# Kernel tuning notes

Measured on AMD Instinct MI355X. Metric: run time of the kernel, lower is better.

The kernel has to match this reference:

```python
import jax, jax.numpy as jnp
import numpy as np

N_NODES = 200000
N_EVENTS = 150000
MEM_DIM = 128
RAW_DIM = 128
TIME_DIM = 128
MSG_DIM = 2 * MEM_DIM + RAW_DIM + TIME_DIM  # 512, IdentityMessage out_channels


def setup_inputs() -> dict:
    key = jax.random.key(0)
    ks = jax.random.split(key, 10)
    memory = jax.random.normal(ks[0], (N_NODES, MEM_DIM), jnp.float32)
    last_update = jax.random.randint(ks[1], (N_NODES,), 0, 1000, jnp.int32)
    src = jax.random.randint(ks[2], (N_EVENTS,), 0, N_NODES, jnp.int32)
    dst = jax.random.randint(ks[3], (N_EVENTS,), 0, N_NODES, jnp.int32)
    t = jax.random.randint(ks[4], (N_EVENTS,), 0, 100000, jnp.int32)
    raw_msg = jax.random.normal(ks[5], (N_EVENTS, RAW_DIM), jnp.float32)
    time_w = jax.random.normal(ks[6], (TIME_DIM,), jnp.float32) * 0.05
    time_b = jax.random.normal(ks[7], (TIME_DIM,), jnp.float32) * 0.05
    W_ih = jax.random.normal(ks[8], (3 * MEM_DIM, MSG_DIM), jnp.float32) * (1.0 / np.sqrt(MSG_DIM))
    W_hh = jax.random.normal(ks[9], (3 * MEM_DIM, MEM_DIM), jnp.float32) * (1.0 / np.sqrt(MEM_DIM))
    b_ih = jnp.zeros((3 * MEM_DIM,), jnp.float32)
    b_hh = jnp.zeros((3 * MEM_DIM,), jnp.float32)
    return {"memory": memory, "last_update": last_update, "src": src, "dst": dst,
            "t": t, "raw_msg": raw_msg, "time_w": time_w, "time_b": time_b,
            "W_ih": W_ih, "W_hh": W_hh, "b_ih": b_ih, "b_hh": b_hh}


def reference(memory, last_update, src, dst, t, raw_msg, time_w, time_b, W_ih, W_hh, b_ih, b_hh):
    N = memory.shape[0]

    def compute_msg(s, d):
        # t_rel = t - last_update[src]; time enc = cos(Linear(1->time_dim)(t_rel))
        t_rel = (t - last_update[s]).astype(memory.dtype)
        t_enc = jnp.cos(t_rel[:, None] * time_w[None, :] + time_b[None, :])
        # IdentityMessage: concat(mem[src], mem[dst], raw_msg, t_enc)  -> [E, MSG_DIM]
        return jnp.concatenate([memory[s], memory[d], raw_msg, t_enc], axis=-1)

    msg_s = compute_msg(src, dst)   # source-direction store
    msg_d = compute_msg(dst, src)   # destination-direction store (edges reversed)
    idx = jnp.concatenate([src, dst])          # destination node of each message
    msg = jnp.concatenate([msg_s, msg_d], axis=0)
    tt = jnp.concatenate([t, t])

    # MeanAggregator: segment-mean of messages per destination node
    sums = jax.ops.segment_sum(msg, idx, num_segments=N)
    cnt = jax.ops.segment_sum(jnp.ones_like(tt, dtype=msg.dtype), idx, num_segments=N)
    aggr = sums / jnp.maximum(cnt, 1.0)[:, None]

    # GRUCell(aggr, memory)
    gi = aggr @ W_ih.T + b_ih
    gh = memory @ W_hh.T + b_hh
    i_r, i_z, i_n = jnp.split(gi, 3, axis=-1)
    h_r, h_z, h_n = jnp.split(gh, 3, axis=-1)
    r = jax.nn.sigmoid(i_r + h_r)
    z = jax.nn.sigmoid(i_z + h_z)
    n = jnp.tanh(i_n + r * h_n)
    new_memory = (1.0 - z) * n + z * memory

    # last_update = scatter(t, idx, reduce='max') over all nodes
    new_last_update = jnp.zeros((N,), tt.dtype).at[idx].max(tt)
    return new_memory, new_last_update
```

## Files before the change

kernel.cpp:

```cpp
#include <hip/hip_runtime.h>
#include <cstdint>


#define MEMD 128
#define ACCD 384
#define MSGD 512

typedef __attribute__((ext_vector_type(8))) short bf16x8;
typedef __attribute__((ext_vector_type(2))) short bf16x2;
typedef __attribute__((ext_vector_type(4))) float f32x4;

static __device__ __forceinline__ short f2bf(float f) {
    uint32_t u = __builtin_bit_cast(uint32_t, f);
    u = (u + 0x7FFFu + ((u >> 16) & 1u)) >> 16;
    return (short)u;
}
static __device__ __forceinline__ float bf2f(short s) {
    return __builtin_bit_cast(float, ((uint32_t)(uint16_t)s) << 16);
}
static __device__ __forceinline__ uint32_t pack2bf(float a, float b) {
    return (uint32_t)(uint16_t)f2bf(a) | ((uint32_t)(uint16_t)f2bf(b) << 16);
}

#define GI_SLOTS (24 * 16 * 64)
#define GH_SLOTS (24 * 4 * 64)

__global__ __launch_bounds__(256) void tgn_prep_w(
    const float* __restrict__ W_ih, const float* __restrict__ W_hh,
    bf16x8* __restrict__ Wb)
{
    const int s = blockIdx.x * 256 + threadIdx.x;
    if (s >= GI_SLOTS + GH_SLOTS) return;
    const float* src;
    if (s < GI_SLOTS) {
        const int n = s / (16 * 64), rem = s % (16 * 64);
        const int ks = rem / 64, l = rem % 64;
        const int j = n * 16 + (l & 15), k = ks * 32 + (l >> 4) * 8;
        src = W_ih + (size_t)j * MSGD + k;
    } else {
        const int s2 = s - GI_SLOTS;
        const int n = s2 / (4 * 64), rem = s2 % (4 * 64);
        const int ks = rem / 64, l = rem % 64;
        const int j = n * 16 + (l & 15), k = ks * 32 + (l >> 4) * 8;
        src = W_hh + (size_t)j * MEMD + k;
    }
    bf16x8 v;
    #pragma unroll
    for (int e = 0; e < 8; ++e) v[e] = f2bf(src[e]);
    Wb[s] = v;
}

__global__ __launch_bounds__(256) void tgn_fill(
    const int* __restrict__ src, const int* __restrict__ dst, const int* __restrict__ t,
    int* __restrict__ head, int* __restrict__ nxt, int* __restrict__ lu_new,
    int n_events)
{
    const int e = blockIdx.x * 256 + threadIdx.x;
    if (e >= n_events) return;
    const int s = src[e];
    const int d = dst[e];
    const int te = t[e];
    nxt[2 * e]     = atomicExch(head + s, 2 * e);
    nxt[2 * e + 1] = atomicExch(head + d, 2 * e + 1);
    atomicMax(lu_new + s, te);
    atomicMax(lu_new + d, te);
}

#define WPTR(NN, S) ((S) < 4 ? (Wh + (size_t)((NN) * 4 + (S)) * 64 + lane)      \
                             : (Wb + (size_t)((NN) * 16 + (S) - 4) * 64 + lane))

#define MFMA2(ACCN, BV)                                                          \
    ACCN[0] = __builtin_amdgcn_mfma_f32_16x16x32_bf16(a0, BV, ACCN[0], 0, 0, 0); \
    ACCN[1] = __builtin_amdgcn_mfma_f32_16x16x32_bf16(a1, BV, ACCN[1], 0, 0, 0);

#define STEP(S, B0, B1, B2, ACCARR)                                              \
    {                                                                            \
        const int ks_ = (S) < 4 ? (S) : (S) - 4;                                 \
        const bf16x8 a0 = Xf[(0 * 16 + ks_) * 64 + lane];                        \
        const bf16x8 a1 = Xf[(1 * 16 + ks_) * 64 + lane];                        \
        MFMA2(ACCARR[0], B0)                                                     \
        MFMA2(ACCARR[1], B1)                                                     \
        MFMA2(ACCARR[2], B2)                                                     \
    }                                                                            \
    if ((S) + 3 < 20) {                                                          \
        B0 = *WPTR(n0, (S) + 3);                                                 \
        B1 = *WPTR(n1, (S) + 3);                                                 \
        B2 = *WPTR(n2, (S) + 3);                                                 \
    }

__global__ __launch_bounds__(512, 4) void tgn_gru_fused(
    const float* __restrict__ mem, const int* __restrict__ head,
    const int* __restrict__ nxt,
    const int* __restrict__ src, const int* __restrict__ dst,
    const int* __restrict__ t, const float* __restrict__ raw_msg,
    const int* __restrict__ last_update,
    const float* __restrict__ time_w, const float* __restrict__ time_b,
    const bf16x8* __restrict__ Wb,
    const float* __restrict__ b_ih, const float* __restrict__ b_hh,
    const int* __restrict__ lu, float* __restrict__ out,
    float* __restrict__ out2, int n_nodes)
{
    __shared__ bf16x8 Xf[2 * 16 * 64];
    ushort* Xh = reinterpret_cast<ushort*>(Xf);
    uint32_t* X32 = reinterpret_cast<uint32_t*>(Xf);
    float*  Sout = reinterpret_cast<float*>(Xf);

    const int tid = threadIdx.x;
    const int lane = tid & 63;
    const int wv = tid >> 6;
    const int node0 = blockIdx.x * 32;

    const bf16x8* __restrict__ Wh = Wb + GI_SLOTS;
    const int n0 = wv, n1 = wv + 8, n2 = wv + 16;

    {
        const int m = wv >> 2, ks = wv & 3;
        const int slotbase = (m * 16 + ks) * 64;
        int node = node0 + m * 16 + (lane & 15);
        if (node >= n_nodes) node = n_nodes - 1;
        const int kbase = ks * 32 + (lane >> 4) * 8;
        const float4 pa = *reinterpret_cast<const float4*>(mem + (size_t)node * MEMD + kbase);
        const float4 pb = *reinterpret_cast<const float4*>(mem + (size_t)node * MEMD + kbase + 4);
        bf16x8 xv;
        xv[0] = f2bf(pa.x); xv[1] = f2bf(pa.y); xv[2] = f2bf(pa.z); xv[3] = f2bf(pa.w);
        xv[4] = f2bf(pb.x); xv[5] = f2bf(pb.y); xv[6] = f2bf(pb.z); xv[7] = f2bf(pb.w);
        Xf[slotbase + lane] = xv;
    }

    bf16x8 rA0 = *WPTR(n0, 0), rA1 = *WPTR(n1, 0), rA2 = *WPTR(n2, 0);
    bf16x8 rB0 = *WPTR(n0, 1), rB1 = *WPTR(n1, 1), rB2 = *WPTR(n2, 1);
    bf16x8 rC0 = *WPTR(n0, 2), rC1 = *WPTR(n1, 2), rC2 = *WPTR(n2, 2);

    const int col = lane & 15;
    const int rgrp = lane >> 4;

    uint32_t hmask = 0;
    #pragma unroll
    for (int m = 0; m < 2; ++m)
        #pragma unroll
        for (int r = 0; r < 4; ++r) {
            const int node = node0 + m * 16 + rgrp * 4 + r;
            if (node < n_nodes && head[node] >= 0) hmask |= 1u << (m * 4 + r);
        }

    {
        const int j0 = lane * 2;
        const float2 tw = *reinterpret_cast<const float2*>(time_w + j0);
        const float2 tb = *reinterpret_cast<const float2*>(time_b + j0);
        const int nb = node0 + wv * 4;

        int kq[4];
        float lus[4];
        float A[4][6];
        int C[4];
        #pragma unroll
        for (int q = 0; q < 4; ++q) {
            kq[q] = (nb + q < n_nodes) ? head[nb + q] : -1;
            lus[q] = 0.f;
            C[q] = 0;
            #pragma unroll
            for (int z = 0; z < 6; ++z) A[q][z] = 0.f;
        }
        #pragma unroll
        for (int q = 0; q < 4; ++q)
            if (kq[q] >= 0) lus[q] = (float)last_update[nb + q];

        bool more = (kq[0] >= 0) | (kq[1] >= 0) | (kq[2] >= 0) | (kq[3] >= 0);
        while (more) {
            #pragma unroll
            for (int q = 0; q < 4; ++q) {
                const int k = kq[q];
                if (k >= 0) {
                    kq[q] = nxt[k];
                    const int e = k >> 1;
                    const int other = (k & 1) ? src[e] : dst[e];
                    const float te = (float)t[e];
                    const float2 rw = *reinterpret_cast<const float2*>(raw_msg + (size_t)e * MEMD + j0);
                    const float2 mb = *reinterpret_cast<const float2*>(mem + (size_t)other * MEMD + j0);
                    const float dt = te - lus[q];
                    A[q][4] += __cosf(fmaf(dt, tw.x, tb.x));
                    A[q][5] += __cosf(fmaf(dt, tw.y, tb.y));
                    A[q][2] += rw.x; A[q][3] += rw.y;
                    A[q][0] += mb.x; A[q][1] += mb.y;
                    ++C[q];
                }
            }
            more = (kq[0] >= 0) | (kq[1] >= 0) | (kq[2] >= 0) | (kq[3] >= 0);
        }

        #pragma unroll
        for (int q = 0; q < 4; ++q) {
            if (C[q] > 0) {
                const float inv = 1.0f / (float)C[q];
                const int nn_ = wv * 4 + q;
                const int mn = nn_ >> 4, nif = nn_ & 15;
                #pragma unroll
                for (int p = 0; p < 3; ++p) {
                    const int cc = 128 + p * 128 + j0;
                    const int ks = cc >> 5;
                    const int hi = (cc >> 3) & 3;
                    const int u32idx = ((mn * 16 + ks) * 64 + hi * 16 + nif) * 4 + (lane & 3);
                    X32[u32idx] = pack2bf(A[q][p * 2] * inv, A[q][p * 2 + 1] * inv);
                }
            }
        }
    }

    __syncthreads();

    f32x4 acc_i[3][2], acc_h[3][2];
    #pragma unroll
    for (int c = 0; c < 3; ++c)
        #pragma unroll
        for (int m = 0; m < 2; ++m) {
            acc_i[c][m] = (f32x4){0.f, 0.f, 0.f, 0.f};
            acc_h[c][m] = (f32x4){0.f, 0.f, 0.f, 0.f};
        }

    STEP(0,  rA0, rA1, rA2, acc_h)
    STEP(1,  rB0, rB1, rB2, acc_h)
    STEP(2,  rC0, rC1, rC2, acc_h)
    STEP(3,  rA0, rA1, rA2, acc_h)
    STEP(4,  rB0, rB1, rB2, acc_i)
    STEP(5,  rC0, rC1, rC2, acc_i)
    STEP(6,  rA0, rA1, rA2, acc_i)
    STEP(7,  rB0, rB1, rB2, acc_i)
    STEP(8,  rC0, rC1, rC2, acc_i)
    STEP(9,  rA0, rA1, rA2, acc_i)
    STEP(10, rB0, rB1, rB2, acc_i)
    STEP(11, rC0, rC1, rC2, acc_i)
    STEP(12, rA0, rA1, rA2, acc_i)
    STEP(13, rB0, rB1, rB2, acc_i)
    STEP(14, rC0, rC1, rC2, acc_i)
    STEP(15, rA0, rA1, rA2, acc_i)
    STEP(16, rB0, rB1, rB2, acc_i)
    STEP(17, rC0, rC1, rC2, acc_i)
    STEP(18, rA0, rA1, rA2, acc_i)
    STEP(19, rB0, rB1, rB2, acc_i)

    const int jr = wv * 16 + col;
    const float bir = b_ih[jr], biz = b_ih[jr + 128], bin = b_ih[jr + 256];
    const float bhr = b_hh[jr], bhz = b_hh[jr + 128], bhn = b_hh[jr + 256];
    const int ksj = jr >> 5;
    const int sub = ((jr >> 3) & 3) * 16;
    const int elem = jr & 7;

    float rout[2][4];
    #pragma unroll
    for (int m = 0; m < 2; ++m) {
        #pragma unroll
        for (int r = 0; r < 4; ++r) {
            const bool has = (hmask >> (m * 4 + r)) & 1;
            const float gir = (has ? acc_i[0][m][r] : 0.f) + bir;
            const float giz = (has ? acc_i[1][m][r] : 0.f) + biz;
            const float gin = (has ? acc_i[2][m][r] : 0.f) + bin;
            const float ghr = acc_h[0][m][r] + bhr;
            const float ghz = acc_h[1][m][r] + bhz;
            const float ghn = acc_h[2][m][r] + bhn;
            const float rr = __fdividef(1.0f, 1.0f + __expf(-(gir + ghr)));
            const float zz = __fdividef(1.0f, 1.0f + __expf(-(giz + ghz)));
            const float targ = fmaf(rr, ghn, gin);
            const float e2v = __expf(2.0f * targ);
            const float nn = __fdividef(e2v - 1.0f, e2v + 1.0f);
            const int slot = (m * 16 + ksj) * 64 + sub + (rgrp * 4 + r);
            const float mv = bf2f((short)Xh[slot * 8 + elem]);
            rout[m][r] = (1.0f - zz) * nn + zz * mv;
        }
    }
    if (tid < 32 && node0 + tid < n_nodes) out2[node0 + tid] = (float)lu[node0 + tid];
    __syncthreads();

    #pragma unroll
    for (int m = 0; m < 2; ++m)
        #pragma unroll
        for (int r = 0; r < 4; ++r)
            Sout[(m * 16 + rgrp * 4 + r) * MEMD + jr] = rout[m][r];
    __syncthreads();

    float4* out4 = reinterpret_cast<float4*>(out + (size_t)node0 * MEMD);
    const float4* S4 = reinterpret_cast<const float4*>(Sout);
    if (node0 + 32 <= n_nodes) {
        #pragma unroll
        for (int it = 0; it < 2; ++it)
            out4[it * 512 + tid] = S4[it * 512 + tid];
    } else {
        #pragma unroll
        for (int it = 0; it < 2; ++it) {
            const int idx = it * 512 + tid;
            if (node0 + (idx >> 5) < n_nodes) out4[idx] = S4[idx];
        }
    }
}

extern "C" void kernel_launch(void* const* d_in, const int* in_sizes, int n_in,
                              void* d_out, int out_size, void* d_ws, size_t ws_size,
                              hipStream_t stream)
{
    const float* memory      = (const float*)d_in[0];
    const int*   last_update = (const int*)d_in[1];
    const int*   src         = (const int*)d_in[2];
    const int*   dst         = (const int*)d_in[3];
    const int*   t           = (const int*)d_in[4];
    const float* raw_msg     = (const float*)d_in[5];
    const float* time_w      = (const float*)d_in[6];
    const float* time_b      = (const float*)d_in[7];
    const float* W_ih        = (const float*)d_in[8];
    const float* W_hh        = (const float*)d_in[9];
    const float* b_ih        = (const float*)d_in[10];
    const float* b_hh        = (const float*)d_in[11];

    const int n_nodes  = in_sizes[0] / MEMD;
    const int n_events = in_sizes[2];

    int*   head = (int*)d_ws;
    int*   nxt  = head + n_nodes;
    int*   lu   = nxt + 2 * n_events;
    bf16x8* Wb  = (bf16x8*)(lu + n_nodes);

    (void)hipMemsetAsync(head, 0xFF, (size_t)n_nodes * sizeof(int), stream);
    (void)hipMemsetAsync(lu, 0, (size_t)n_nodes * sizeof(int), stream);

    tgn_prep_w<<<dim3((GI_SLOTS + GH_SLOTS + 255) / 256), dim3(256), 0, stream>>>(W_ih, W_hh, Wb);

    tgn_fill<<<dim3((n_events + 255) / 256), dim3(256), 0, stream>>>(
        src, dst, t, head, nxt, lu, n_events);

    float* out2 = (float*)d_out + (size_t)n_nodes * MEMD;
    tgn_gru_fused<<<dim3((n_nodes + 31) / 32), dim3(512), 0, stream>>>(
        memory, head, nxt, src, dst, t, raw_msg, last_update, time_w, time_b,
        Wb, b_ih, b_hh, lu, (float*)d_out, out2, n_nodes);
}
```

Before: 303.5 us.

## Halve nodes per block to 16 and drop register-pipelined weight prefetch

Each block now handles 16 nodes instead of 32: half the shared memory, two linked-list walkers per wave instead of four, and a single M-tile per MFMA. The hand-unrolled 3-deep weight prefetch pipeline is replaced by plain unrolled loops that load weights just before use. Launch bounds rise to 6 blocks per CU to raise occupancy and hide the latency of the irregular gather. In exchange every weight fragment is fetched twice as often per node, which adds L2 traffic, and the explicit prefetch overlap is lost.

```diff
diff --git a/kernel.cpp b/kernel.cpp
--- a/kernel.cpp
+++ b/kernel.cpp
@@ -66,29 +66,7 @@
     atomicMax(lu_new + d, te);
 }
 
-#define WPTR(NN, S) ((S) < 4 ? (Wh + (size_t)((NN) * 4 + (S)) * 64 + lane)      \
-                             : (Wb + (size_t)((NN) * 16 + (S) - 4) * 64 + lane))
-
-#define MFMA2(ACCN, BV)                                                          \
-    ACCN[0] = __builtin_amdgcn_mfma_f32_16x16x32_bf16(a0, BV, ACCN[0], 0, 0, 0); \
-    ACCN[1] = __builtin_amdgcn_mfma_f32_16x16x32_bf16(a1, BV, ACCN[1], 0, 0, 0);
-
-#define STEP(S, B0, B1, B2, ACCARR)                                              \
-    {                                                                            \
-        const int ks_ = (S) < 4 ? (S) : (S) - 4;                                 \
-        const bf16x8 a0 = Xf[(0 * 16 + ks_) * 64 + lane];                        \
-        const bf16x8 a1 = Xf[(1 * 16 + ks_) * 64 + lane];                        \
-        MFMA2(ACCARR[0], B0)                                                     \
-        MFMA2(ACCARR[1], B1)                                                     \
-        MFMA2(ACCARR[2], B2)                                                     \
-    }                                                                            \
-    if ((S) + 3 < 20) {                                                          \
-        B0 = *WPTR(n0, (S) + 3);                                                 \
-        B1 = *WPTR(n1, (S) + 3);                                                 \
-        B2 = *WPTR(n2, (S) + 3);                                                 \
-    }
-
-__global__ __launch_bounds__(512, 4) void tgn_gru_fused(
+__global__ __launch_bounds__(512, 6) void tgn_gru_fused(
     const float* __restrict__ mem, const int* __restrict__ head,
     const int* __restrict__ nxt,
     const int* __restrict__ src, const int* __restrict__ dst,
@@ -100,7 +78,7 @@
     const int* __restrict__ lu, float* __restrict__ out,
     float* __restrict__ out2, int n_nodes)
 {
-    __shared__ bf16x8 Xf[2 * 16 * 64];
+    __shared__ bf16x8 Xf[16 * 64];
     ushort* Xh = reinterpret_cast<ushort*>(Xf);
     uint32_t* X32 = reinterpret_cast<uint32_t*>(Xf);
     float*  Sout = reinterpret_cast<float*>(Xf);
@@ -108,53 +86,51 @@
     const int tid = threadIdx.x;
     const int lane = tid & 63;
     const int wv = tid >> 6;
-    const int node0 = blockIdx.x * 32;
+    const int node0 = blockIdx.x * 16;
 
     const bf16x8* __restrict__ Wh = Wb + GI_SLOTS;
     const int n0 = wv, n1 = wv + 8, n2 = wv + 16;
 
-    {
-        const int m = wv >> 2, ks = wv & 3;
-        const int slotbase = (m * 16 + ks) * 64;
-        int node = node0 + m * 16 + (lane & 15);
-        if (node >= n_nodes) node = n_nodes - 1;
-        const int kbase = ks * 32 + (lane >> 4) * 8;
-        const float4 pa = *reinterpret_cast<const float4*>(mem + (size_t)node * MEMD + kbase);
-        const float4 pb = *reinterpret_cast<const float4*>(mem + (size_t)node * MEMD + kbase + 4);
-        bf16x8 xv;
-        xv[0] = f2bf(pa.x); xv[1] = f2bf(pa.y); xv[2] = f2bf(pa.z); xv[3] = f2bf(pa.w);
-        xv[4] = f2bf(pb.x); xv[5] = f2bf(pb.y); xv[6] = f2bf(pb.z); xv[7] = f2bf(pb.w);
-        Xf[slotbase + lane] = xv;
-    }
-
-    bf16x8 rA0 = *WPTR(n0, 0), rA1 = *WPTR(n1, 0), rA2 = *WPTR(n2, 0);
-    bf16x8 rB0 = *WPTR(n0, 1), rB1 = *WPTR(n1, 1), rB2 = *WPTR(n2, 1);
-    bf16x8 rC0 = *WPTR(n0, 2), rC1 = *WPTR(n1, 2), rC2 = *WPTR(n2, 2);
+    #pragma unroll
+    for (int i = 0; i < 2; ++i) {
+        const int slot = i * 512 + tid;
+        const int l = slot & 63;
+        const int ks = (slot >> 6) & 15;
+        if (ks < 4) {
+            int node = node0 + (l & 15);
+            if (node >= n_nodes) node = n_nodes - 1;
+            const int kbase = ks * 32 + (l >> 4) * 8;
+            const float4 pa = *reinterpret_cast<const float4*>(mem + (size_t)node * MEMD + kbase);
+            const float4 pb = *reinterpret_cast<const float4*>(mem + (size_t)node * MEMD + kbase + 4);
+            bf16x8 xv;
+            xv[0] = f2bf(pa.x); xv[1] = f2bf(pa.y); xv[2] = f2bf(pa.z); xv[3] = f2bf(pa.w);
+            xv[4] = f2bf(pb.x); xv[5] = f2bf(pb.y); xv[6] = f2bf(pb.z); xv[7] = f2bf(pb.w);
+            Xf[slot] = xv;
+        }
+    }
 
     const int col = lane & 15;
     const int rgrp = lane >> 4;
 
     uint32_t hmask = 0;
     #pragma unroll
-    for (int m = 0; m < 2; ++m)
-        #pragma unroll
-        for (int r = 0; r < 4; ++r) {
-            const int node = node0 + m * 16 + rgrp * 4 + r;
-            if (node < n_nodes && head[node] >= 0) hmask |= 1u << (m * 4 + r);
-        }
+    for (int r = 0; r < 4; ++r) {
+        const int node = node0 + rgrp * 4 + r;
+        if (node < n_nodes && head[node] >= 0) hmask |= 1u << r;
+    }
 
     {
         const int j0 = lane * 2;
         const float2 tw = *reinterpret_cast<const float2*>(time_w + j0);
         const float2 tb = *reinterpret_cast<const float2*>(time_b + j0);
-        const int nb = node0 + wv * 4;
-
-        int kq[4];
-        float lus[4];
-        float A[4][6];
-        int C[4];
+        const int nb = node0 + wv * 2;
+
+        int kq[2];
+        float lus[2];
+        float A[2][6];
+        int C[2];
         #pragma unroll
-        for (int q = 0; q < 4; ++q) {
+        for (int q = 0; q < 2; ++q) {
             kq[q] = (nb + q < n_nodes) ? head[nb + q] : -1;
             lus[q] = 0.f;
             C[q] = 0;
@@ -162,13 +138,13 @@
             for (int z = 0; z < 6; ++z) A[q][z] = 0.f;
         }
         #pragma unroll
-        for (int q = 0; q < 4; ++q)
+        for (int q = 0; q < 2; ++q)
             if (kq[q] >= 0) lus[q] = (float)last_update[nb + q];
 
-        bool more = (kq[0] >= 0) | (kq[1] >= 0) | (kq[2] >= 0) | (kq[3] >= 0);
+        bool more = (kq[0] >= 0) | (kq[1] >= 0);
         while (more) {
             #pragma unroll
-            for (int q = 0; q < 4; ++q) {
+            for (int q = 0; q < 2; ++q) {
                 const int k = kq[q];
                 if (k >= 0) {
                     kq[q] = nxt[k];
@@ -185,21 +161,20 @@
                     ++C[q];
                 }
             }
-            more = (kq[0] >= 0) | (kq[1] >= 0) | (kq[2] >= 0) | (kq[3] >= 0);
+            more = (kq[0] >= 0) | (kq[1] >= 0);
         }
 
         #pragma unroll
-        for (int q = 0; q < 4; ++q) {
+        for (int q = 0; q < 2; ++q) {
             if (C[q] > 0) {
                 const float inv = 1.0f / (float)C[q];
-                const int nn_ = wv * 4 + q;
-                const int mn = nn_ >> 4, nif = nn_ & 15;
+                const int nif = wv * 2 + q;
                 #pragma unroll
                 for (int p = 0; p < 3; ++p) {
                     const int cc = 128 + p * 128 + j0;
                     const int ks = cc >> 5;
                     const int hi = (cc >> 3) & 3;
-                    const int u32idx = ((mn * 16 + ks) * 64 + hi * 16 + nif) * 4 + (lane & 3);
+                    const int u32idx = (ks * 64 + hi * 16 + nif) * 4 + (lane & 3);
                     X32[u32idx] = pack2bf(A[q][p * 2] * inv, A[q][p * 2 + 1] * inv);
                 }
             }
@@ -208,35 +183,39 @@
 
     __syncthreads();
 
-    f32x4 acc_i[3][2], acc_h[3][2];
-    #pragma unroll
-    for (int c = 0; c < 3; ++c)
-        #pragma unroll
-        for (int m = 0; m < 2; ++m) {
-            acc_i[c][m] = (f32x4){0.f, 0.f, 0.f, 0.f};
-            acc_h[c][m] = (f32x4){0.f, 0.f, 0.f, 0.f};
-        }
-
-    STEP(0,  rA0, rA1, rA2, acc_h)
-    STEP(1,  rB0, rB1, rB2, acc_h)
-    STEP(2,  rC0, rC1, rC2, acc_h)
-    STEP(3,  rA0, rA1, rA2, acc_h)
-    STEP(4,  rB0, rB1, rB2, acc_i)
-    STEP(5,  rC0, rC1, rC2, acc_i)
-    STEP(6,  rA0, rA1, rA2, acc_i)
-    STEP(7,  rB0, rB1, rB2, acc_i)
-    STEP(8,  rC0, rC1, rC2, acc_i)
-    STEP(9,  rA0, rA1, rA2, acc_i)
-    STEP(10, rB0, rB1, rB2, acc_i)
-    STEP(11, rC0, rC1, rC2, acc_i)
-    STEP(12, rA0, rA1, rA2, acc_i)
-    STEP(13, rB0, rB1, rB2, acc_i)
-    STEP(14, rC0, rC1, rC2, acc_i)
-    STEP(15, rA0, rA1, rA2, acc_i)
-    STEP(16, rB0, rB1, rB2, acc_i)
-    STEP(17, rC0, rC1, rC2, acc_i)
-    STEP(18, rA0, rA1, rA2, acc_i)
-    STEP(19, rB0, rB1, rB2, acc_i)
+    f32x4 acc_i[3], acc_h[3];
+    #pragma unroll
+    for (int c = 0; c < 3; ++c) {
+        acc_i[c] = (f32x4){0.f, 0.f, 0.f, 0.f};
+        acc_h[c] = (f32x4){0.f, 0.f, 0.f, 0.f};
+    }
+
+    #pragma unroll
+    for (int ks = 0; ks < 4; ++ks) {
+        const bf16x8 bh0 = Wh[(size_t)(n0 * 4 + ks) * 64 + lane];
+        const bf16x8 bh1 = Wh[(size_t)(n1 * 4 + ks) * 64 + lane];
+        const bf16x8 bh2 = Wh[(size_t)(n2 * 4 + ks) * 64 + lane];
+        const bf16x8 bi0 = Wb[(size_t)(n0 * 16 + ks) * 64 + lane];
+        const bf16x8 bi1 = Wb[(size_t)(n1 * 16 + ks) * 64 + lane];
+        const bf16x8 bi2 = Wb[(size_t)(n2 * 16 + ks) * 64 + lane];
+        const bf16x8 a0 = Xf[ks * 64 + lane];
+        acc_h[0] = __builtin_amdgcn_mfma_f32_16x16x32_bf16(a0, bh0, acc_h[0], 0, 0, 0);
+        acc_h[1] = __builtin_amdgcn_mfma_f32_16x16x32_bf16(a0, bh1, acc_h[1], 0, 0, 0);
+        acc_h[2] = __builtin_amdgcn_mfma_f32_16x16x32_bf16(a0, bh2, acc_h[2], 0, 0, 0);
+        acc_i[0] = __builtin_amdgcn_mfma_f32_16x16x32_bf16(a0, bi0, acc_i[0], 0, 0, 0);
+        acc_i[1] = __builtin_amdgcn_mfma_f32_16x16x32_bf16(a0, bi1, acc_i[1], 0, 0, 0);
+        acc_i[2] = __builtin_amdgcn_mfma_f32_16x16x32_bf16(a0, bi2, acc_i[2], 0, 0, 0);
+    }
+    #pragma unroll
+    for (int ks = 4; ks < 16; ++ks) {
+        const bf16x8 bi0 = Wb[(size_t)(n0 * 16 + ks) * 64 + lane];
+        const bf16x8 bi1 = Wb[(size_t)(n1 * 16 + ks) * 64 + lane];
+        const bf16x8 bi2 = Wb[(size_t)(n2 * 16 + ks) * 64 + lane];
+        const bf16x8 a0 = Xf[ks * 64 + lane];
+        acc_i[0] = __builtin_amdgcn_mfma_f32_16x16x32_bf16(a0, bi0, acc_i[0], 0, 0, 0);
+        acc_i[1] = __builtin_amdgcn_mfma_f32_16x16x32_bf16(a0, bi1, acc_i[1], 0, 0, 0);
+        acc_i[2] = __builtin_amdgcn_mfma_f32_16x16x32_bf16(a0, bi2, acc_i[2], 0, 0, 0);
+    }
 
     const int jr = wv * 16 + col;
     const float bir = b_ih[jr], biz = b_ih[jr + 128], bin = b_ih[jr + 256];
@@ -245,50 +224,39 @@
     const int sub = ((jr >> 3) & 3) * 16;
     const int elem = jr & 7;
 
-    float rout[2][4];
-    #pragma unroll
-    for (int m = 0; m < 2; ++m) {
-        #pragma unroll
-        for (int r = 0; r < 4; ++r) {
-            const bool has = (hmask >> (m * 4 + r)) & 1;
-            const float gir = (has ? acc_i[0][m][r] : 0.f) + bir;
-            const float giz = (has ? acc_i[1][m][r] : 0.f) + biz;
-            const float gin = (has ? acc_i[2][m][r] : 0.f) + bin;
-            const float ghr = acc_h[0][m][r] + bhr;
-            const float ghz = acc_h[1][m][r] + bhz;
-            const float ghn = acc_h[2][m][r] + bhn;
-            const float rr = __fdividef(1.0f, 1.0f + __expf(-(gir + ghr)));
-            const float zz = __fdividef(1.0f, 1.0f + __expf(-(giz + ghz)));
-            const float targ = fmaf(rr, ghn, gin);
-            const float e2v = __expf(2.0f * targ);
-            const float nn = __fdividef(e2v - 1.0f, e2v + 1.0f);
-            const int slot = (m * 16 + ksj) * 64 + sub + (rgrp * 4 + r);
-            const float mv = bf2f((short)Xh[slot * 8 + elem]);
-            rout[m][r] = (1.0f - zz) * nn + zz * mv;
-        }
-    }
-    if (tid < 32 && node0 + tid < n_nodes) out2[node0 + tid] = (float)lu[node0 + tid];
+    float rout[4];
+    #pragma unroll
+    for (int r = 0; r < 4; ++r) {
+        const bool has = (hmask >> r) & 1;
+        const float gir = (has ? acc_i[0][r] : 0.f) + bir;
+        const float giz = (has ? acc_i[1][r] : 0.f) + biz;
+        const float gin = (has ? acc_i[2][r] : 0.f) + bin;
+        const float ghr = acc_h[0][r] + bhr;
+        const float ghz = acc_h[1][r] + bhz;
+        const float ghn = acc_h[2][r] + bhn;
+        const float rr = __fdividef(1.0f, 1.0f + __expf(-(gir + ghr)));
+        const float zz = __fdividef(1.0f, 1.0f + __expf(-(giz + ghz)));
+        const float targ = fmaf(rr, ghn, gin);
+        const float e2v = __expf(2.0f * targ);
+        const float nn = __fdividef(e2v - 1.0f, e2v + 1.0f);
+        const int slot = ksj * 64 + sub + (rgrp * 4 + r);
+        const float mv = bf2f((short)Xh[slot * 8 + elem]);
+        rout[r] = (1.0f - zz) * nn + zz * mv;
+    }
+    if (tid < 16 && node0 + tid < n_nodes) out2[node0 + tid] = (float)lu[node0 + tid];
     __syncthreads();
 
     #pragma unroll
-    for (int m = 0; m < 2; ++m)
-        #pragma unroll
-        for (int r = 0; r < 4; ++r)
-            Sout[(m * 16 + rgrp * 4 + r) * MEMD + jr] = rout[m][r];
+    for (int r = 0; r < 4; ++r)
+        Sout[(rgrp * 4 + r) * MEMD + jr] = rout[r];
     __syncthreads();
 
     float4* out4 = reinterpret_cast<float4*>(out + (size_t)node0 * MEMD);
     const float4* S4 = reinterpret_cast<const float4*>(Sout);
-    if (node0 + 32 <= n_nodes) {
-        #pragma unroll
-        for (int it = 0; it < 2; ++it)
-            out4[it * 512 + tid] = S4[it * 512 + tid];
+    if (node0 + 16 <= n_nodes) {
+        out4[tid] = S4[tid];
     } else {
-        #pragma unroll
-        for (int it = 0; it < 2; ++it) {
-            const int idx = it * 512 + tid;
-            if (node0 + (idx >> 5) < n_nodes) out4[idx] = S4[idx];
-        }
+        if (node0 + (tid >> 5) < n_nodes) out4[tid] = S4[tid];
     }
 }
 
@@ -326,7 +294,7 @@
         src, dst, t, head, nxt, lu, n_events);
 
     float* out2 = (float*)d_out + (size_t)n_nodes * MEMD;
-    tgn_gru_fused<<<dim3((n_nodes + 31) / 32), dim3(512), 0, stream>>>(
+    tgn_gru_fused<<<dim3((n_nodes + 15) / 16), dim3(512), 0, stream>>>(
         memory, head, nxt, src, dst, t, raw_msg, last_update, time_w, time_b,
         Wb, b_ih, b_hh, lu, (float*)d_out, out2, n_nodes);
 }
```

Measured after the change: 365.7 us. 20.5% more time.
